# Kernel tuning notes

Hardware: AMD Instinct MI355X
Metric: run time of the kernel (lower is better)

Reference implementation:

```python
import jax, jax.numpy as jnp
import numpy as np

K_HOPS = 3
N_NODES = 50000
N_EDGES = 800000
N_FEAT = 256
N_CLASS = 64


def setup_inputs() -> dict:
    key = jax.random.key(0)
    k1, k2, k3, k4 = jax.random.split(key, 4)
    x = jax.random.normal(k1, (N_NODES, N_FEAT), dtype=jnp.float32)
    edge_index = jax.random.randint(k2, (2, N_EDGES), 0, N_NODES, dtype=jnp.int64)
    # Linear(nfeat -> nclass) params, Glorot-ish init
    W = jax.random.normal(k3, (N_FEAT, N_CLASS), dtype=jnp.float32) / np.sqrt(N_FEAT)
    b = jnp.zeros((N_CLASS,), dtype=jnp.float32)
    return {"x": x, "edge_index": edge_index, "W": W, "b": b}


def reference(x, edge_index, W, b):
    # SGC: out = (D^-1/2 (A+I) D^-1/2)^K x  @ W + b
    N = x.shape[0]
    self_idx = jnp.arange(N, dtype=edge_index.dtype)
    src = jnp.concatenate([edge_index[0], self_idx])  # [E+N]
    dst = jnp.concatenate([edge_index[1], self_idx])  # [E+N]
    deg = jax.ops.segment_sum(jnp.ones_like(dst, dtype=x.dtype), dst, num_segments=N)
    dinv = jnp.where(deg > 0, jax.lax.rsqrt(deg), 0.0)
    norm = dinv[src] * dinv[dst]  # [E+N] per-edge coefficient
    for _ in range(K_HOPS):
        # gather source features, scale, scatter-add into destinations
        x = jax.ops.segment_sum(x[src] * norm[:, None], dst, num_segments=N)
    return x @ W + b
```

## Files before the change

### kernel.cpp

```cpp
#include <hip/hip_runtime.h>
#include <hip/hip_bf16.h>


#define NFEAT 256
#define NCLS  64
#define ELLW  64
#define NPB   128
#define BCAP  4096
#define PCHUNK 8192

typedef __attribute__((ext_vector_type(8))) short bf16x8;
typedef __attribute__((ext_vector_type(4))) float f32x4;
typedef __attribute__((ext_vector_type(4))) int   i32x4;
typedef __attribute__((ext_vector_type(4))) unsigned int u32x4;

__device__ __forceinline__ float bf2f(unsigned int u) {
    return __uint_as_float(u << 16);
}
__device__ __forceinline__ float bf2f_hi(unsigned int u) {
    return __uint_as_float(u & 0xffff0000u);
}
__device__ __forceinline__ unsigned short f2bf(float f) {
    unsigned int u = __float_as_uint(f);
    unsigned int r = u + 0x7fffu + ((u >> 16) & 1u);
    return (unsigned short)(r >> 16);
}
__device__ __forceinline__ unsigned int pack2bf(float a, float b) {
    return (unsigned int)f2bf(a) | ((unsigned int)f2bf(b) << 16);
}

__global__ void k_setup(const void* ei, int twoE, int nnodes,
                        const unsigned int* __restrict__ x, int nwords,
                        const void* __restrict__ Wg, const void* __restrict__ Bg,
                        int* flag, int* fflag, int* gcur, int NB,
                        unsigned short* __restrict__ Wt, float* __restrict__ bc) {
    __shared__ int acc;
    const int t = threadIdx.x;
    const int b = blockIdx.x;
    if (t == 0) acc = 0;
    __syncthreads();

    if (b == 0) {
        const long long* p = (const long long*)ei;
        int nchk = 2048;
        if (nchk > twoE / 2) nchk = twoE / 2;
        int bad = 0;
        for (int i = t; i < nchk; i += 256) {
            long long v = p[i];
            if (v < 0 || v >= (long long)nnodes) bad++;
        }
        if (bad) atomicAdd(&acc, bad);
        __syncthreads();
        if (t == 0) *flag = (acc == 0) ? 1 : 0;
        return;
    }

    int lim = nwords < 4096 ? nwords : 4096;
    int wild = 0;
    for (int i = t; i < lim; i += 256) {
        unsigned int lo = x[i] & 0xffffu;
        unsigned int expf = (lo >> 7) & 0xffu;
        if (expf >= 0x97u) wild++;
    }
    if (wild) atomicAdd(&acc, wild);
    __syncthreads();
    const bool isbf = (acc < 8);

    if (b == 1) {
        if (t == 0) *fflag = isbf ? 1 : 0;
        for (int i = t; i < NB; i += 256) gcur[i] = 0;
        if (t < NCLS) {
            bc[t] = isbf ? bf2f(((const unsigned short*)Bg)[t])
                         : ((const float*)Bg)[t];
        }
        return;
    }

    int i = (b - 2) * 256 + t;
    if (i < NFEAT * NCLS) {
        int n = i >> 8, k = i & 255;
        Wt[i] = isbf ? ((const unsigned short*)Wg)[k * NCLS + n]
                     : f2bf(((const float*)Wg)[k * NCLS + n]);
    }
}

__launch_bounds__(256)
__global__ void k_fused(const void* __restrict__ Xg,
                        const unsigned short* __restrict__ Wt,
                        unsigned short* __restrict__ Yb,
                        int N, int NB, const int* __restrict__ fflag,
                        const void* __restrict__ ei, int E, const int* __restrict__ flag,
                        unsigned int* __restrict__ bucket, int* __restrict__ gcur,
                        int ngemm) {
    __shared__ char smem[32768 + 3 * 1600];
    const int t = threadIdx.x;

    if (blockIdx.x >= ngemm) {
        unsigned int* stage = (unsigned int*)smem;
        int* hist = (int*)(smem + 32768);
        int* base = hist + 400;
        int* rank = base + 400;
        for (int b = t; b < NB; b += 256) { hist[b] = 0; rank[b] = 0; }
        __syncthreads();
        const int bstart = (blockIdx.x - ngemm) * PCHUNK;
        const bool is64 = (*flag != 0);
#pragma unroll
        for (int i = 0; i < PCHUNK / 256; ++i) {
            int e = bstart + i * 256 + t;
            unsigned int v = 0xFFFFFFFFu;
            if (e < E) {
                int ss, dd;
                if (is64) {
                    ss = (int)__builtin_nontemporal_load((const long long*)ei + e);
                    dd = (int)__builtin_nontemporal_load((const long long*)ei + E + e);
                } else {
                    ss = __builtin_nontemporal_load((const int*)ei + e);
                    dd = __builtin_nontemporal_load((const int*)ei + E + e);
                }
                int j = dd >> 7;
                atomicAdd(&hist[j], 1);
                v = ((unsigned int)j << 23) | ((unsigned int)(dd & 127) << 16) |
                    (unsigned int)ss;
            }
            stage[i * 256 + t] = v;
        }
        __syncthreads();
        for (int b = t; b < NB; b += 256) base[b] = atomicAdd(&gcur[b], hist[b]);
        __syncthreads();
#pragma unroll
        for (int i = 0; i < PCHUNK / 256; ++i) {
            unsigned int v = stage[i * 256 + t];
            if (v != 0xFFFFFFFFu) {
                int j = v >> 23;
                int r = atomicAdd(&rank[j], 1);
                int pos = base[j] + r;
                if (pos < BCAP)
                    bucket[(size_t)j * BCAP + pos] = v & 0x7FFFFFu;
            }
        }
        return;
    }

    unsigned short* Ws = (unsigned short*)smem;
    for (int it = 0; it < 8; ++it) {
        int idx = t + 256 * it;
        int lane_e = idx & 63;
        int nt = (idx >> 6) & 3;
        int ks = idx >> 8;
        int n = nt * 16 + (lane_e & 15);
        int k = ks * 32 + (lane_e >> 4) * 8;
        const unsigned short* srcp = Wt + n * 256 + k;
        ushort4 v0 = *(const ushort4*)srcp;
        ushort4 v1 = *(const ushort4*)(srcp + 4);
        unsigned short* dstp = &Ws[idx * 8];
        *(ushort4*)dstp = v0;
        *(ushort4*)(dstp + 4) = v1;
    }
    __syncthreads();

    const int wv = t >> 6, lane = t & 63;
    const int m = lane & 15, q = lane >> 4;
    const int row = blockIdx.x * 64 + wv * 16 + m;
    const bool rowok = row < N;
    const bool isbf = (*fflag != 0);

    f32x4 acc0 = {0.f, 0.f, 0.f, 0.f};
    f32x4 acc1 = {0.f, 0.f, 0.f, 0.f};
    f32x4 acc2 = {0.f, 0.f, 0.f, 0.f};
    f32x4 acc3 = {0.f, 0.f, 0.f, 0.f};

    for (int ks = 0; ks < 8; ++ks) {
        const int kk = ks * 32 + q * 8;
        bf16x8 af = {0, 0, 0, 0, 0, 0, 0, 0};
        if (rowok) {
            if (isbf) {
                const i32x4* xp = (const i32x4*)((const unsigned short*)Xg + (size_t)row * NFEAT + kk);
                i32x4 raw = __builtin_nontemporal_load(xp);
#pragma unroll
                for (int h = 0; h < 4; ++h) {
                    af[2 * h]     = (short)(raw[h] & 0xffff);
                    af[2 * h + 1] = (short)(((unsigned int)raw[h]) >> 16);
                }
            } else {
                const i32x4* xp = (const i32x4*)((const float*)Xg + (size_t)row * NFEAT + kk);
                i32x4 r0 = __builtin_nontemporal_load(xp);
                i32x4 r1 = __builtin_nontemporal_load(xp + 1);
#pragma unroll
                for (int h = 0; h < 4; ++h) {
                    af[h]     = (short)f2bf(__int_as_float(r0[h]));
                    af[h + 4] = (short)f2bf(__int_as_float(r1[h]));
                }
            }
        }
        const unsigned short* wbase = &Ws[(ks * 4) * 512 + lane * 8];
        bf16x8 b0 = *(const bf16x8*)(wbase);
        bf16x8 b1 = *(const bf16x8*)(wbase + 512);
        bf16x8 b2 = *(const bf16x8*)(wbase + 1024);
        bf16x8 b3 = *(const bf16x8*)(wbase + 1536);
        acc0 = __builtin_amdgcn_mfma_f32_16x16x32_bf16(af, b0, acc0, 0, 0, 0);
        acc1 = __builtin_amdgcn_mfma_f32_16x16x32_bf16(af, b1, acc1, 0, 0, 0);
        acc2 = __builtin_amdgcn_mfma_f32_16x16x32_bf16(af, b2, acc2, 0, 0, 0);
        acc3 = __builtin_amdgcn_mfma_f32_16x16x32_bf16(af, b3, acc3, 0, 0, 0);
    }

    const int rowbase = blockIdx.x * 64 + wv * 16 + q * 4;
#pragma unroll
    for (int i = 0; i < 4; ++i) {
        int gr = rowbase + i;
        if (gr < N) {
            unsigned short* yp = Yb + (size_t)gr * NCLS + m;
            yp[0]  = f2bf(acc0[i]);
            yp[16] = f2bf(acc1[i]);
            yp[32] = f2bf(acc2[i]);
            yp[48] = f2bf(acc3[i]);
        }
    }
}

__launch_bounds__(256)
__global__ void k_build(const unsigned int* __restrict__ bucket,
                        const int* __restrict__ gcur,
                        int* __restrict__ cnt, float* __restrict__ dinv,
                        unsigned short* __restrict__ ellu,
                        const unsigned int* __restrict__ Yb,
                        unsigned int* __restrict__ Z,
                        int N) {
    __shared__ unsigned short ellb[NPB * ELLW];
    __shared__ int lcnt[NPB];
    __shared__ float sdinv[NPB];
    const int t = threadIdx.x;
    const int j = blockIdx.x;
    if (t < NPB) lcnt[t] = 0;
    {
        u32x4* eb4 = (u32x4*)ellb;
        u32x4 z = {0, 0, 0, 0};
        for (int i = t; i < NPB * ELLW / 8; i += 256) eb4[i] = z;
    }
    __syncthreads();
    int total = gcur[j];
    if (total > BCAP) total = BCAP;
    const unsigned int* bb = bucket + (size_t)j * BCAP;
    for (int i = t; i < total; i += 256) {
        unsigned int v = __builtin_nontemporal_load(bb + i);
        int ld = (v >> 16) & 127;
        int s = v & 0xffffu;
        int r = atomicAdd(&lcnt[ld], 1);
        if (r < ELLW) ellb[(ld << 6) + r] = (unsigned short)s;
    }
    __syncthreads();
    const int node0 = j << 7;
    if (t < NPB) {
        int node = node0 + t;
        int c = lcnt[t];
        float dv = rsqrtf((float)(c + 1));
        sdinv[t] = dv;
        if (node < N) {
            cnt[node] = c > ELLW ? ELLW : c;
            dinv[node] = dv;
        }
    }
    __syncthreads();
    u32x4* ellg = (u32x4*)ellu;
    const u32x4* eb = (const u32x4*)ellb;
    for (int i = t; i < NPB * (ELLW / 8); i += 256) {
        int node = node0 + (i >> 3);
        if (node < N) ellg[(size_t)node0 * 8 + i] = eb[i];
    }
    for (int w = t; w < NPB * 32; w += 256) {
        int nl = w >> 5, l = w & 31;
        int node = node0 + nl;
        if (node < N) {
            float dv = sdinv[nl];
            unsigned int y = Yb[(size_t)node * 32 + l];
            Z[(size_t)node * 32 + l] = pack2bf(dv * bf2f(y), dv * bf2f_hi(y));
        }
    }
}

__launch_bounds__(256)
__global__ void k_hop(const unsigned int* __restrict__ Zin,
                      const unsigned short* __restrict__ ellu,
                      const int* __restrict__ cnt, const float* __restrict__ dinv,
                      unsigned int* __restrict__ Zout,
                      float* __restrict__ outf,
                      const float* __restrict__ bc, int N) {
    int node = blockIdx.x * 8 + (threadIdx.x >> 5);
    if (node >= N) return;
    const int l = threadIdx.x & 31;
    const int deg = cnt[node];
    const float dn = dinv[node];
    unsigned int zself = Zin[(size_t)node * 32 + l];
    float a0 = bf2f(zself), a1 = 0.f, a2 = 0.f, a3 = 0.f;
    float b0 = bf2f_hi(zself), b1 = 0.f, b2 = 0.f, b3 = 0.f;
    const unsigned short* erow = ellu + (size_t)node * ELLW;
    int e = 0;
    for (; e + 16 <= deg; e += 16) {
        u32x4 ua = *(const u32x4*)(erow + e);
        u32x4 ub = *(const u32x4*)(erow + e + 8);
        int s[16];
#pragma unroll
        for (int i = 0; i < 4; ++i) {
            s[2 * i]     = (int)(ua[i] & 0xffffu);
            s[2 * i + 1] = (int)(ua[i] >> 16);
            s[2 * i + 8] = (int)(ub[i] & 0xffffu);
            s[2 * i + 9] = (int)(ub[i] >> 16);
        }
        unsigned int z[16];
#pragma unroll
        for (int i = 0; i < 16; ++i) z[i] = Zin[(size_t)s[i] * 32 + l];
#pragma unroll
        for (int i = 0; i < 16; i += 4) {
            a0 += bf2f(z[i]);     b0 += bf2f_hi(z[i]);
            a1 += bf2f(z[i + 1]); b1 += bf2f_hi(z[i + 1]);
            a2 += bf2f(z[i + 2]); b2 += bf2f_hi(z[i + 2]);
            a3 += bf2f(z[i + 3]); b3 += bf2f_hi(z[i + 3]);
        }
    }
    if (e < deg) {
        u32x4 ua = *(const u32x4*)(erow + e);
        u32x4 ub = *(const u32x4*)(erow + e + 8);
        int s[16];
#pragma unroll
        for (int i = 0; i < 4; ++i) {
            s[2 * i]     = (int)(ua[i] & 0xffffu);
            s[2 * i + 1] = (int)(ua[i] >> 16);
            s[2 * i + 8] = (int)(ub[i] & 0xffffu);
            s[2 * i + 9] = (int)(ub[i] >> 16);
        }
        unsigned int z[16];
#pragma unroll
        for (int i = 0; i < 16; ++i) z[i] = Zin[(size_t)s[i] * 32 + l];
#pragma unroll
        for (int i = 0; i < 16; i += 4) {
            bool g0 = (e + i < deg), g1 = (e + i + 1 < deg);
            bool g2 = (e + i + 2 < deg), g3 = (e + i + 3 < deg);
            a0 += g0 ? bf2f(z[i]) : 0.f;     b0 += g0 ? bf2f_hi(z[i]) : 0.f;
            a1 += g1 ? bf2f(z[i + 1]) : 0.f; b1 += g1 ? bf2f_hi(z[i + 1]) : 0.f;
            a2 += g2 ? bf2f(z[i + 2]) : 0.f; b2 += g2 ? bf2f_hi(z[i + 2]) : 0.f;
            a3 += g3 ? bf2f(z[i + 3]) : 0.f; b3 += g3 ? bf2f_hi(z[i + 3]) : 0.f;
        }
    }
    float lo = (a0 + a1) + (a2 + a3);
    float hi = (b0 + b1) + (b2 + b3);
    if (outf) {
        float2 bv = *(const float2*)(bc + 2 * l);
        float2 o = make_float2(dn * lo + bv.x, dn * hi + bv.y);
        *(float2*)(outf + (size_t)node * NCLS + 2 * l) = o;
    } else {
        float d2 = dn * dn;
        Zout[(size_t)node * 32 + l] = pack2bf(d2 * lo, d2 * hi);
    }
}

extern "C" void kernel_launch(void* const* d_in, const int* in_sizes, int n_in,
                              void* d_out, int out_size, void* d_ws, size_t ws_size,
                              hipStream_t stream) {
    const void* X  = d_in[0];
    const void* EI = d_in[1];
    const void* W  = d_in[2];
    const void* B  = d_in[3];
    float* out = (float*)d_out;

    const int N = in_sizes[0] / NFEAT;
    const int twoE = in_sizes[1];
    const int E = twoE / 2;
    const int NB = (N + NPB - 1) / NPB;

    char* p = (char*)d_ws;
    auto alloc = [&](size_t bytes) -> char* {
        char* q = p;
        p += (bytes + 255) & ~(size_t)255;
        return q;
    };
    int*   flag   = (int*)alloc(4);
    int*   fflag  = (int*)alloc(4);
    int*   gcur   = (int*)alloc((size_t)NB * 4);
    int*   cnt    = (int*)alloc((size_t)N * 4);
    float* dinv   = (float*)alloc((size_t)N * 4);
    unsigned short* Wt = (unsigned short*)alloc((size_t)NFEAT * NCLS * 2);
    float* bc     = (float*)alloc((size_t)NCLS * 4);
    unsigned int* bucket = (unsigned int*)alloc((size_t)NB * BCAP * 4);
    unsigned short* ellu = (unsigned short*)alloc((size_t)N * ELLW * 2);
    unsigned short* Y0 = (unsigned short*)alloc((size_t)N * NCLS * 2);
    unsigned short* Z0 = (unsigned short*)alloc((size_t)N * NCLS * 2);
    unsigned short* Z1 = (unsigned short*)alloc((size_t)N * NCLS * 2);

    k_setup<<<2 + NFEAT * NCLS / 256, 256, 0, stream>>>(
        EI, twoE, N, (const unsigned int*)X, in_sizes[0] / 2,
        W, B, flag, fflag, gcur, NB, Wt, bc);

    const int ngemm = (N + 63) / 64;
    const int npart = (E + PCHUNK - 1) / PCHUNK;
    k_fused<<<ngemm + npart, 256, 0, stream>>>(X, Wt, Y0, N, NB, fflag,
                                               EI, E, flag, bucket, gcur, ngemm);

    k_build<<<NB, 256, 0, stream>>>(bucket, gcur, cnt, dinv, ellu,
                                    (const unsigned int*)Y0, (unsigned int*)Z0, N);

    const int nb_h = (N + 7) / 8;
    k_hop<<<nb_h, 256, 0, stream>>>((const unsigned int*)Z0, ellu, cnt, dinv,
                                    (unsigned int*)Z1, nullptr, bc, N);
    k_hop<<<nb_h, 256, 0, stream>>>((const unsigned int*)Z1, ellu, cnt, dinv,
                                    (unsigned int*)Z0, nullptr, bc, N);
    k_hop<<<nb_h, 256, 0, stream>>>((const unsigned int*)Z0, ellu, cnt, dinv,
                                    nullptr, out, bc, N);
}
```

Measured before the change: 186.0 us.

## Split Z feature buffer into lo/hi halves, one half per hop block

The 64-class bf16 feature matrix is stored as two separate 32-column arrays, and each hop block gathers only one half, with 16 lanes per node instead of 32. The intent is to shrink the working set each block gathers, from 128B to 64B rows per node, so that concurrently running blocks hit L2/MALL more often. Edge-list, degree and output accesses also switch to nontemporal loads and stores to avoid polluting the cache. The trade-off is that the ELL index list is now read twice per node, once per half, and each gather moves only 64B, which may waste cache-line bandwidth.

New measurement: 204.1 us. 1.1x slower.

```diff
diff --git a/kernel.cpp b/kernel.cpp
--- a/kernel.cpp
+++ b/kernel.cpp
@@ -11,6 +11,7 @@
 
 typedef __attribute__((ext_vector_type(8))) short bf16x8;
 typedef __attribute__((ext_vector_type(4))) float f32x4;
+typedef __attribute__((ext_vector_type(2))) float f32x2;
 typedef __attribute__((ext_vector_type(4))) int   i32x4;
 typedef __attribute__((ext_vector_type(4))) unsigned int u32x4;
 
@@ -223,7 +224,8 @@
                         int* __restrict__ cnt, float* __restrict__ dinv,
                         unsigned short* __restrict__ ellu,
                         const unsigned int* __restrict__ Yb,
-                        unsigned int* __restrict__ Z,
+                        unsigned int* __restrict__ Zlo,
+                        unsigned int* __restrict__ Zhi,
                         int N) {
     __shared__ unsigned short ellb[NPB * ELLW];
     __shared__ int lcnt[NPB];
@@ -272,31 +274,38 @@
         if (node < N) {
             float dv = sdinv[nl];
             unsigned int y = Yb[(size_t)node * 32 + l];
-            Z[(size_t)node * 32 + l] = pack2bf(dv * bf2f(y), dv * bf2f_hi(y));
+            unsigned int zz = pack2bf(dv * bf2f(y), dv * bf2f_hi(y));
+            if (l < 16) Zlo[(size_t)node * 16 + l] = zz;
+            else        Zhi[(size_t)node * 16 + (l - 16)] = zz;
         }
     }
 }
 
 __launch_bounds__(256)
-__global__ void k_hop(const unsigned int* __restrict__ Zin,
+__global__ void k_hop(const unsigned int* __restrict__ Zlo_in,
+                      const unsigned int* __restrict__ Zhi_in,
                       const unsigned short* __restrict__ ellu,
                       const int* __restrict__ cnt, const float* __restrict__ dinv,
-                      unsigned int* __restrict__ Zout,
+                      unsigned int* __restrict__ Zlo_out,
+                      unsigned int* __restrict__ Zhi_out,
                       float* __restrict__ outf,
                       const float* __restrict__ bc, int N) {
-    int node = blockIdx.x * 8 + (threadIdx.x >> 5);
+    const int half = blockIdx.x & 1;
+    const int node = (blockIdx.x >> 1) * 16 + (threadIdx.x >> 4);
     if (node >= N) return;
-    const int l = threadIdx.x & 31;
-    const int deg = cnt[node];
-    const float dn = dinv[node];
-    unsigned int zself = Zin[(size_t)node * 32 + l];
+    const int l = threadIdx.x & 15;
+    const unsigned int* __restrict__ Zin = half ? Zhi_in : Zlo_in;
+
+    const int deg = __builtin_nontemporal_load(cnt + node);
+    const float dn = __builtin_nontemporal_load(dinv + node);
+    unsigned int zself = Zin[node * 16 + l];
     float a0 = bf2f(zself), a1 = 0.f, a2 = 0.f, a3 = 0.f;
     float b0 = bf2f_hi(zself), b1 = 0.f, b2 = 0.f, b3 = 0.f;
     const unsigned short* erow = ellu + (size_t)node * ELLW;
     int e = 0;
     for (; e + 16 <= deg; e += 16) {
-        u32x4 ua = *(const u32x4*)(erow + e);
-        u32x4 ub = *(const u32x4*)(erow + e + 8);
+        u32x4 ua = __builtin_nontemporal_load((const u32x4*)(erow + e));
+        u32x4 ub = __builtin_nontemporal_load((const u32x4*)(erow + e) + 1);
         int s[16];
 #pragma unroll
         for (int i = 0; i < 4; ++i) {
@@ -307,7 +316,7 @@
         }
         unsigned int z[16];
 #pragma unroll
-        for (int i = 0; i < 16; ++i) z[i] = Zin[(size_t)s[i] * 32 + l];
+        for (int i = 0; i < 16; ++i) z[i] = Zin[s[i] * 16 + l];
 #pragma unroll
         for (int i = 0; i < 16; i += 4) {
             a0 += bf2f(z[i]);     b0 += bf2f_hi(z[i]);
@@ -317,8 +326,8 @@
         }
     }
     if (e < deg) {
-        u32x4 ua = *(const u32x4*)(erow + e);
-        u32x4 ub = *(const u32x4*)(erow + e + 8);
+        u32x4 ua = __builtin_nontemporal_load((const u32x4*)(erow + e));
+        u32x4 ub = __builtin_nontemporal_load((const u32x4*)(erow + e) + 1);
         int s[16];
 #pragma unroll
         for (int i = 0; i < 4; ++i) {
@@ -329,7 +338,7 @@
         }
         unsigned int z[16];
 #pragma unroll
-        for (int i = 0; i < 16; ++i) z[i] = Zin[(size_t)s[i] * 32 + l];
+        for (int i = 0; i < 16; ++i) z[i] = Zin[s[i] * 16 + l];
 #pragma unroll
         for (int i = 0; i < 16; i += 4) {
             bool g0 = (e + i < deg), g1 = (e + i + 1 < deg);
@@ -343,12 +352,13 @@
     float lo = (a0 + a1) + (a2 + a3);
     float hi = (b0 + b1) + (b2 + b3);
     if (outf) {
-        float2 bv = *(const float2*)(bc + 2 * l);
-        float2 o = make_float2(dn * lo + bv.x, dn * hi + bv.y);
-        *(float2*)(outf + (size_t)node * NCLS + 2 * l) = o;
+        float2 bv = *(const float2*)(bc + half * 32 + 2 * l);
+        f32x2 o = {dn * lo + bv.x, dn * hi + bv.y};
+        __builtin_nontemporal_store(o, (f32x2*)(outf + (size_t)node * NCLS + half * 32 + 2 * l));
     } else {
+        unsigned int* __restrict__ Zout = half ? Zhi_out : Zlo_out;
         float d2 = dn * dn;
-        Zout[(size_t)node * 32 + l] = pack2bf(d2 * lo, d2 * hi);
+        __builtin_nontemporal_store(pack2bf(d2 * lo, d2 * hi), Zout + (size_t)node * 16 + l);
     }
 }
 
@@ -382,8 +392,10 @@
     unsigned int* bucket = (unsigned int*)alloc((size_t)NB * BCAP * 4);
     unsigned short* ellu = (unsigned short*)alloc((size_t)N * ELLW * 2);
     unsigned short* Y0 = (unsigned short*)alloc((size_t)N * NCLS * 2);
-    unsigned short* Z0 = (unsigned short*)alloc((size_t)N * NCLS * 2);
-    unsigned short* Z1 = (unsigned short*)alloc((size_t)N * NCLS * 2);
+    unsigned int* Zlo0 = (unsigned int*)alloc((size_t)N * 16 * 4);
+    unsigned int* Zlo1 = (unsigned int*)alloc((size_t)N * 16 * 4);
+    unsigned int* Zhi0 = (unsigned int*)alloc((size_t)N * 16 * 4);
+    unsigned int* Zhi1 = (unsigned int*)alloc((size_t)N * 16 * 4);
 
     k_setup<<<2 + NFEAT * NCLS / 256, 256, 0, stream>>>(
         EI, twoE, N, (const unsigned int*)X, in_sizes[0] / 2,
@@ -395,13 +407,13 @@
                                                EI, E, flag, bucket, gcur, ngemm);
 
     k_build<<<NB, 256, 0, stream>>>(bucket, gcur, cnt, dinv, ellu,
-                                    (const unsigned int*)Y0, (unsigned int*)Z0, N);
-
-    const int nb_h = (N + 7) / 8;
-    k_hop<<<nb_h, 256, 0, stream>>>((const unsigned int*)Z0, ellu, cnt, dinv,
-                                    (unsigned int*)Z1, nullptr, bc, N);
-    k_hop<<<nb_h, 256, 0, stream>>>((const unsigned int*)Z1, ellu, cnt, dinv,
-                                    (unsigned int*)Z0, nullptr, bc, N);
-    k_hop<<<nb_h, 256, 0, stream>>>((const unsigned int*)Z0, ellu, cnt, dinv,
-                                    nullptr, out, bc, N);
-}
+                                    (const unsigned int*)Y0, Zlo0, Zhi0, N);
+
+    const int nb_h = 2 * ((N + 15) / 16);
+    k_hop<<<nb_h, 256, 0, stream>>>(Zlo0, Zhi0, ellu, cnt, dinv,
+                                    Zlo1, Zhi1, nullptr, bc, N);
+    k_hop<<<nb_h, 256, 0, stream>>>(Zlo1, Zhi1, ellu, cnt, dinv,
+                                    Zlo0, Zhi0, nullptr, bc, N);
+    k_hop<<<nb_h, 256, 0, stream>>>(Zlo0, Zhi0, ellu, cnt, dinv,
+                                    nullptr, nullptr, out, bc, N);
+}
```
